# Optimization experiments

Measured on AMD Instinct MI355X. Metric: run time of the kernel, lower is better.

The kernel has to match this reference:

```python
import jax, jax.numpy as jnp
import numpy as np

N = 262144   # number of samples
C = 16       # GMM components
D = 64       # feature dim


def setup_inputs() -> dict:
    key = jax.random.key(0)
    k1, k2, k3, k4 = jax.random.split(key, 4)
    inputs = jax.random.normal(k1, (N, D), dtype=jnp.float32)
    # SPD inverse covariances, as produced by inverting fitted GMM covariances
    R = jax.random.normal(k2, (C, D, D), dtype=jnp.float32)
    covariances_inv = jnp.einsum('cij,ckj->cik', R, R) / D + 0.1 * jnp.eye(D, dtype=jnp.float32)
    means = jax.random.normal(k3, (C, D), dtype=jnp.float32)
    w = jax.random.uniform(k4, (C,), dtype=jnp.float32, minval=0.1, maxval=1.0)
    weights = w / jnp.sum(w)  # mixture weights sum to 1
    return {"inputs": inputs, "covariances_inv": covariances_inv,
            "means": means, "weights": weights}


def reference(inputs, covariances_inv, means, weights):
    # Mahalanobis quadratic form per component: d[n,c] = (x_n - m_c)^T Sigma_c^{-1} (x_n - m_c)
    centered = inputs[:, None, :] - means[None, :, :]                # [N, C, D]
    distances_sqr = jnp.einsum('ncd,cde,nce->nc', centered, covariances_inv, centered)  # [N, C]
    # score_n = prod_c d[n,c] ** w_c
    score = jnp.prod(distances_sqr ** weights[None, :], axis=1)      # [N]
    return score
```

## Files before the change

### kernel.cpp

```cpp
#include <hip/hip_runtime.h>

typedef __attribute__((ext_vector_type(4))) float f32x4;
typedef __attribute__((ext_vector_type(8))) short bf16x8;

__device__ __forceinline__ short f2bf(float f) {
    union { float f; unsigned u; } v; v.f = f;
    unsigned u = v.u + 0x7FFFu + ((v.u >> 16) & 1u);
    return (short)(u >> 16);
}
__device__ __forceinline__ int pack_bf2(float a, float b) {
    union { float f; unsigned u; } ua, ub; ua.f = a; ub.f = b;
    unsigned x = ua.u + 0x8000u, y = ub.u + 0x8000u;
    return (int)__builtin_amdgcn_perm(y, x, 0x07060302u);
}
__device__ __forceinline__ float bflo(int p) {
    union { int i; float f; } v; v.i = p << 16; return v.f;
}
__device__ __forceinline__ float bfhi(int p) {
    union { int i; float f; } v; v.i = p & 0xffff0000; return v.f;
}

#if __has_builtin(__builtin_amdgcn_permlane16_swap) && \
    __has_builtin(__builtin_amdgcn_permlane32_swap)
__device__ __forceinline__ float quad_sum(float dp) {
    unsigned u = __float_as_uint(dp);
    auto r1 = __builtin_amdgcn_permlane16_swap(u, u, false, false);
    float s = __uint_as_float(r1[0]) + __uint_as_float(r1[1]);
    unsigned v = __float_as_uint(s);
    auto r2 = __builtin_amdgcn_permlane32_swap(v, v, false, false);
    return __uint_as_float(r2[0]) + __uint_as_float(r2[1]);
}
#else
__device__ __forceinline__ float quad_sum(float dp) {
    dp += __shfl_xor(dp, 16, 64);
    dp += __shfl_xor(dp, 32, 64);
    return dp;
}
#endif

__global__ void gmm_prep(const float* __restrict__ Ainv,
                         const float* __restrict__ means,
                         short* __restrict__ AbP16,
                         float* __restrict__ biasP,
                         float* __restrict__ kscal) {
    __shared__ float sA[64 * 68];
    __shared__ float sm[64];
    __shared__ float sb[64];
    const int c = blockIdx.x, t = threadIdx.x;
    const float* A = Ainv + c * 4096;
    #pragma unroll
    for (int i = 0; i < 4; ++i) {
        int flat = i * 1024 + t * 4;
        int r = flat >> 6, col = flat & 63;
        *(f32x4*)&sA[r * 68 + col] = *(const f32x4*)(A + flat);
    }
    if (t < 64) sm[t] = means[c * 64 + t];
    __syncthreads();
    {
        int j = t >> 2, seg = t & 3;
        float p = 0.f;
        #pragma unroll
        for (int k = 0; k < 16; ++k) p += sA[j * 68 + seg * 16 + k] * sm[seg * 16 + k];
        p += __shfl_xor(p, 1, 64); p += __shfl_xor(p, 2, 64);
        if ((t & 3) == 0) sb[j] = p;
    }
    __syncthreads();
    if (t < 64) {
        float km = sm[t] * sb[t];
        #pragma unroll
        for (int off = 32; off >= 1; off >>= 1) km += __shfl_xor(km, off, 64);
        if (t == 0) kscal[c] = km;
        int rt = t >> 4, qh = (t >> 2) & 3, r = t & 3;
        int pj = (rt >> 1) * 32 + 8 * qh + 4 * (rt & 1) + r;
        biasP[c * 64 + t] = -2.f * sb[pj];
    }
    #pragma unroll
    for (int rep = 0; rep < 2; ++rep) {
        int f = rep * 256 + t;
        int rt = f >> 7, kc = (f >> 6) & 1, L = f & 63;
        int ln = L & 15, q = L >> 4;
        int pj = (rt >> 1) * 32 + 8 * (ln >> 2) + 4 * (rt & 1) + (ln & 3);
        const float* src = &sA[pj * 68 + 32 * kc + 8 * q];
        bf16x8 v;
        #pragma unroll
        for (int j = 0; j < 8; ++j) v[j] = f2bf(src[j]);
        *(bf16x8*)(AbP16 + c * 4096 + f * 8) = v;
    }
}

union BFrag { bf16x8 v; int i[4]; };

__global__ __launch_bounds__(256, 4) void gmm_main(
    const float* __restrict__ X,
    const float* __restrict__ weights,
    const short* __restrict__ AbP16,
    const float* __restrict__ biasP,
    const float* __restrict__ kscal,
    float* __restrict__ out) {

    const int tid = threadIdx.x;
    const int lane = tid & 63, w = tid >> 6;
    const int q = lane >> 4, ln = lane & 15;
    const int base = blockIdx.x * 256 + w * 64;

    BFrag xb[4][2];
    #pragma unroll
    for (int t = 0; t < 4; ++t) {
        const float* xr = X + (size_t)(base + t * 16 + ln) * 64 + 8 * q;
        #pragma unroll
        for (int kc = 0; kc < 2; ++kc) {
            f32x4 a = *(const f32x4*)(xr + 32 * kc);
            f32x4 b = *(const f32x4*)(xr + 32 * kc + 4);
            xb[t][kc].i[0] = pack_bf2(a[0], a[1]);
            xb[t][kc].i[1] = pack_bf2(a[2], a[3]);
            xb[t][kc].i[2] = pack_bf2(b[0], b[1]);
            xb[t][kc].i[3] = pack_bf2(b[2], b[3]);
        }
    }

    float slog[4] = {0.f, 0.f, 0.f, 0.f};

    #pragma unroll 1
    for (int c = 0; c < 16; ++c) {
        const short* aP = AbP16 + c * 4096 + lane * 8;
        bf16x8 af[8];
        #pragma unroll
        for (int f = 0; f < 8; ++f)
            af[f] = *(const bf16x8*)(aP + f * 512);
        f32x4 bias[4];
        #pragma unroll
        for (int rt = 0; rt < 4; ++rt)
            bias[rt] = *(const f32x4*)(biasP + c * 64 + rt * 16 + q * 4);
        const float kc_ = kscal[c], wcc = weights[c];

        #pragma unroll
        for (int t = 0; t < 4; ++t) {
            float dp0 = 0.f, dp1 = 0.f;
            #pragma unroll
            for (int rt = 0; rt < 4; ++rt) {
                f32x4 acc = __builtin_amdgcn_mfma_f32_16x16x32_bf16(
                    af[rt * 2 + 0], xb[t][0].v, bias[rt], 0, 0, 0);
                acc = __builtin_amdgcn_mfma_f32_16x16x32_bf16(
                    af[rt * 2 + 1], xb[t][1].v, acc, 0, 0, 0);
                int pa = xb[t][rt >> 1].i[(rt & 1) * 2];
                int pb = xb[t][rt >> 1].i[(rt & 1) * 2 + 1];
                float pr = acc[0] * bflo(pa) + acc[1] * bfhi(pa)
                         + acc[2] * bflo(pb) + acc[3] * bfhi(pb);
                if (rt & 1) dp1 += pr; else dp0 += pr;
            }
            float dp = quad_sum(dp0 + dp1);
            float d = fmaxf(dp + kc_, 1e-30f);
            slog[t] = fmaf(wcc, __builtin_amdgcn_logf(d), slog[t]);
        }
    }

    float s0 = (q & 1) ? slog[1] : slog[0];
    float s1 = (q & 1) ? slog[3] : slog[2];
    float sv = (q & 2) ? s1 : s0;
    out[base + lane] = __builtin_amdgcn_exp2f(sv);
}

extern "C" void kernel_launch(void* const* d_in, const int* in_sizes, int n_in,
                              void* d_out, int out_size, void* d_ws, size_t ws_size,
                              hipStream_t stream) {
    const float* X       = (const float*)d_in[0];
    const float* Ainv    = (const float*)d_in[1];
    const float* means   = (const float*)d_in[2];
    const float* weights = (const float*)d_in[3];
    float* out = (float*)d_out;
    const int N = in_sizes[0] / 64;

    short* AbP16 = (short*)d_ws;
    float* biasP = (float*)((char*)d_ws + 131072);
    float* kscal = (float*)((char*)d_ws + 135168);

    gmm_prep<<<dim3(16), dim3(256), 0, stream>>>(Ainv, means, AbP16, biasP, kscal);
    gmm_main<<<dim3(N / 256), dim3(256), 0, stream>>>(X, weights, AbP16, biasP, kscal, out);
}
```

Baseline: 128.8 us.

## Cholesky-factor inverse covariances and compute distance as squared norm

The prep kernel now Cholesky-factors each inverse covariance in shared memory. The main kernel computes y = L^T x - L^T m with MFMA and sums y squared, which replaces the x^T A x product and the separate constant term. The triangular structure lets it skip two of the eight MFMAs per component and tile, and drop the packed-bf16 unpacking of x. The cost is a serial 64-step Cholesky with two barriers per step in the prep kernel, and the numerics change because the triangular factor is rounded to bf16.

```diff
diff --git a/kernel.cpp b/kernel.cpp
--- a/kernel.cpp
+++ b/kernel.cpp
@@ -12,12 +12,6 @@
     union { float f; unsigned u; } ua, ub; ua.f = a; ub.f = b;
     unsigned x = ua.u + 0x8000u, y = ub.u + 0x8000u;
     return (int)__builtin_amdgcn_perm(y, x, 0x07060302u);
-}
-__device__ __forceinline__ float bflo(int p) {
-    union { int i; float f; } v; v.i = p << 16; return v.f;
-}
-__device__ __forceinline__ float bfhi(int p) {
-    union { int i; float f; } v; v.i = p & 0xffff0000; return v.f;
 }
 
 #if __has_builtin(__builtin_amdgcn_permlane16_swap) && \
@@ -41,12 +35,12 @@
 __global__ void gmm_prep(const float* __restrict__ Ainv,
                          const float* __restrict__ means,
                          short* __restrict__ AbP16,
-                         float* __restrict__ biasP,
-                         float* __restrict__ kscal) {
+                         float* __restrict__ biasP) {
     __shared__ float sA[64 * 68];
     __shared__ float sm[64];
     __shared__ float sb[64];
     const int c = blockIdx.x, t = threadIdx.x;
+    const int w4 = t >> 6;
     const float* A = Ainv + c * 4096;
     #pragma unroll
     for (int i = 0; i < 4; ++i) {
@@ -56,23 +50,43 @@
     }
     if (t < 64) sm[t] = means[c * 64 + t];
     __syncthreads();
+
+    for (int k = 0; k < 64; ++k) {
+        if (t < 64) {
+            float Lkk = __builtin_sqrtf(sA[k * 68 + k]);
+            float inv = 1.f / Lkk;
+            if (t == k)      sA[k * 68 + k] = Lkk;
+            else if (t > k)  sA[t * 68 + k] *= inv;
+        }
+        __syncthreads();
+        {
+            int j = t & 63;
+            if (j > k) {
+                float ljk = sA[j * 68 + k];
+                for (int i = k + 1 + w4; i <= j; i += 4)
+                    sA[j * 68 + i] -= ljk * sA[i * 68 + k];
+            }
+        }
+        __syncthreads();
+    }
+
     {
         int j = t >> 2, seg = t & 3;
         float p = 0.f;
         #pragma unroll
-        for (int k = 0; k < 16; ++k) p += sA[j * 68 + seg * 16 + k] * sm[seg * 16 + k];
+        for (int k2 = 0; k2 < 16; ++k2) {
+            int k = seg * 16 + k2;
+            float Mv = (k >= j) ? sA[k * 68 + j] : 0.f;
+            p += Mv * sm[k];
+        }
         p += __shfl_xor(p, 1, 64); p += __shfl_xor(p, 2, 64);
-        if ((t & 3) == 0) sb[j] = p;
+        if (seg == 0) sb[j] = p;
     }
     __syncthreads();
     if (t < 64) {
-        float km = sm[t] * sb[t];
-        #pragma unroll
-        for (int off = 32; off >= 1; off >>= 1) km += __shfl_xor(km, off, 64);
-        if (t == 0) kscal[c] = km;
         int rt = t >> 4, qh = (t >> 2) & 3, r = t & 3;
         int pj = (rt >> 1) * 32 + 8 * qh + 4 * (rt & 1) + r;
-        biasP[c * 64 + t] = -2.f * sb[pj];
+        biasP[c * 64 + t] = -sb[pj];
     }
     #pragma unroll
     for (int rep = 0; rep < 2; ++rep) {
@@ -80,10 +94,14 @@
         int rt = f >> 7, kc = (f >> 6) & 1, L = f & 63;
         int ln = L & 15, q = L >> 4;
         int pj = (rt >> 1) * 32 + 8 * (ln >> 2) + 4 * (rt & 1) + (ln & 3);
-        const float* src = &sA[pj * 68 + 32 * kc + 8 * q];
+        int kbase = 32 * kc + 8 * q;
         bf16x8 v;
         #pragma unroll
-        for (int j = 0; j < 8; ++j) v[j] = f2bf(src[j]);
+        for (int j = 0; j < 8; ++j) {
+            int kk = kbase + j;
+            float x = (kk >= pj) ? sA[kk * 68 + pj] : 0.f;
+            v[j] = f2bf(x);
+        }
         *(bf16x8*)(AbP16 + c * 4096 + f * 8) = v;
     }
 }
@@ -95,7 +113,6 @@
     const float* __restrict__ weights,
     const short* __restrict__ AbP16,
     const float* __restrict__ biasP,
-    const float* __restrict__ kscal,
     float* __restrict__ out) {
 
     const int tid = threadIdx.x;
@@ -123,33 +140,38 @@
     #pragma unroll 1
     for (int c = 0; c < 16; ++c) {
         const short* aP = AbP16 + c * 4096 + lane * 8;
-        bf16x8 af[8];
-        #pragma unroll
-        for (int f = 0; f < 8; ++f)
-            af[f] = *(const bf16x8*)(aP + f * 512);
+        bf16x8 af0 = *(const bf16x8*)(aP + 0 * 512);
+        bf16x8 af1 = *(const bf16x8*)(aP + 1 * 512);
+        bf16x8 af2 = *(const bf16x8*)(aP + 2 * 512);
+        bf16x8 af3 = *(const bf16x8*)(aP + 3 * 512);
+        bf16x8 af5 = *(const bf16x8*)(aP + 5 * 512);
+        bf16x8 af7 = *(const bf16x8*)(aP + 7 * 512);
         f32x4 bias[4];
         #pragma unroll
         for (int rt = 0; rt < 4; ++rt)
             bias[rt] = *(const f32x4*)(biasP + c * 64 + rt * 16 + q * 4);
-        const float kc_ = kscal[c], wcc = weights[c];
+        const float wcc = weights[c];
 
         #pragma unroll
         for (int t = 0; t < 4; ++t) {
-            float dp0 = 0.f, dp1 = 0.f;
+            f32x4 a0 = __builtin_amdgcn_mfma_f32_16x16x32_bf16(af0, xb[t][0].v, bias[0], 0, 0, 0);
+            a0 = __builtin_amdgcn_mfma_f32_16x16x32_bf16(af1, xb[t][1].v, a0, 0, 0, 0);
+            f32x4 a1 = __builtin_amdgcn_mfma_f32_16x16x32_bf16(af2, xb[t][0].v, bias[1], 0, 0, 0);
+            a1 = __builtin_amdgcn_mfma_f32_16x16x32_bf16(af3, xb[t][1].v, a1, 0, 0, 0);
+            f32x4 a2 = __builtin_amdgcn_mfma_f32_16x16x32_bf16(af5, xb[t][1].v, bias[2], 0, 0, 0);
+            f32x4 a3 = __builtin_amdgcn_mfma_f32_16x16x32_bf16(af7, xb[t][1].v, bias[3], 0, 0, 0);
+
+            float dp0 = a0[0] * a0[0], dp1 = a1[0] * a1[0];
+            float dp2 = a2[0] * a2[0], dp3 = a3[0] * a3[0];
             #pragma unroll
-            for (int rt = 0; rt < 4; ++rt) {
-                f32x4 acc = __builtin_amdgcn_mfma_f32_16x16x32_bf16(
-                    af[rt * 2 + 0], xb[t][0].v, bias[rt], 0, 0, 0);
-                acc = __builtin_amdgcn_mfma_f32_16x16x32_bf16(
-                    af[rt * 2 + 1], xb[t][1].v, acc, 0, 0, 0);
-                int pa = xb[t][rt >> 1].i[(rt & 1) * 2];
-                int pb = xb[t][rt >> 1].i[(rt & 1) * 2 + 1];
-                float pr = acc[0] * bflo(pa) + acc[1] * bfhi(pa)
-                         + acc[2] * bflo(pb) + acc[3] * bfhi(pb);
-                if (rt & 1) dp1 += pr; else dp0 += pr;
+            for (int i = 1; i < 4; ++i) {
+                dp0 = fmaf(a0[i], a0[i], dp0);
+                dp1 = fmaf(a1[i], a1[i], dp1);
+                dp2 = fmaf(a2[i], a2[i], dp2);
+                dp3 = fmaf(a3[i], a3[i], dp3);
             }
-            float dp = quad_sum(dp0 + dp1);
-            float d = fmaxf(dp + kc_, 1e-30f);
+            float dp = quad_sum((dp0 + dp1) + (dp2 + dp3));
+            float d = fmaxf(dp, 1e-30f);
             slog[t] = fmaf(wcc, __builtin_amdgcn_logf(d), slog[t]);
         }
     }
@@ -172,8 +194,7 @@
 
     short* AbP16 = (short*)d_ws;
     float* biasP = (float*)((char*)d_ws + 131072);
-    float* kscal = (float*)((char*)d_ws + 135168);
-
-    gmm_prep<<<dim3(16), dim3(256), 0, stream>>>(Ainv, means, AbP16, biasP, kscal);
-    gmm_main<<<dim3(N / 256), dim3(256), 0, stream>>>(X, weights, AbP16, biasP, kscal, out);
-}
+
+    gmm_prep<<<dim3(16), dim3(256), 0, stream>>>(Ainv, means, AbP16, biasP);
+    gmm_main<<<dim3(N / 256), dim3(256), 0, stream>>>(X, weights, AbP16, biasP, out);
+}
```

New measurement: 163.4 us. +26.8%, slower.
